# Optimization experiments

Hardware: AMD Instinct MI355X
Metric: run time of the kernel (lower is better)

Reference implementation:

```python
import jax, jax.numpy as jnp
import numpy as np

FEATURES_DIM = 100000
NUM_FIELDS = 39
EMBED_DIM = 64
DIM_INT = (2, 3)
RANK = (32, 32)
BATCH = 8192


def setup_inputs() -> dict:
    key = jax.random.key(0)
    ks = jax.random.split(key, 6)
    x = jax.random.randint(ks[0], (BATCH, NUM_FIELDS), 0, FEATURES_DIM)
    embed_table = jax.random.normal(ks[1], (FEATURES_DIM, EMBED_DIM), dtype=jnp.float32) * 0.01
    linear_w = jax.random.normal(ks[2], (FEATURES_DIM, 1), dtype=jnp.float32) * 0.01
    linear_bias = jnp.zeros((1,), dtype=jnp.float32)
    # trunc_normal_(std=0.01) approximated by clipped normal
    W0 = jnp.clip(jax.random.normal(ks[3], (DIM_INT[0], RANK[0], NUM_FIELDS), dtype=jnp.float32) * 0.01, -0.02, 0.02)
    W1 = jnp.clip(jax.random.normal(ks[4], (DIM_INT[1], RANK[1], NUM_FIELDS), dtype=jnp.float32) * 0.01, -0.02, 0.02)
    return {"x": x, "embed_table": embed_table, "linear_w": linear_w,
            "linear_bias": linear_bias, "W0": W0, "W1": W1}


def _calc_cross(W, emb):
    # W: (l, j, k) = (dim_int, rank, num_fields); emb: (b, k, i) = (batch, fields, embed)
    # dot_products[b,i,j,l] = sum_k W[l,j,k] * emb[b,k,i]
    dp = jnp.einsum('ljk,bki->bijl', W, emb)          # (b, embed, rank, dim_int)
    prod_over_l = jnp.prod(dp, axis=3)                # (b, embed, rank)
    return jnp.sum(prod_over_l, axis=(1, 2))          # (b,)


def reference(x, embed_table, linear_w, linear_bias, W0, W1):
    emb = embed_table[x]                              # (b, fields, embed)
    lin = jnp.sum(linear_w[x], axis=1) + linear_bias  # (b, 1)
    ret = lin[:, 0] + _calc_cross(W0, emb) + _calc_cross(W1, emb)
    return ret                                        # (b,)
```

## Files before the change

### kernel.cpp

```cpp
#include <hip/hip_runtime.h>
#include <hip/hip_bf16.h>

#define BATCH    8192
#define NF       39
#define ED       64
#define RANK     32
#define KST      72
#define NFRAG    15

typedef _Float16 half8  __attribute__((ext_vector_type(8)));
typedef float    f32x16 __attribute__((ext_vector_type(16)));

__global__ void prep_w(const float* __restrict__ W0,
                       const float* __restrict__ W1,
                       half8* __restrict__ wsW) {
    int d = blockIdx.x * 256 + threadIdx.x;
    if (d >= NFRAG * 64) return;
    int fid  = d >> 6;
    int lane = d & 63;
    int l = fid / 3, kc = fid % 3;
    int j = lane & 31, kh = lane >> 5;
    const float* base = (l < 2) ? (W0 + (l * RANK + j) * NF)
                                : (W1 + ((l - 2) * RANK + j) * NF);
    half8 h;
#pragma unroll
    for (int e = 0; e < 8; ++e) {
        int k = kc * 16 + kh * 8 + e;
        h[e] = (k < NF) ? (_Float16)base[k] : (_Float16)0.0f;
    }
    wsW[d] = h;
}

__global__ __launch_bounds__(256, 3) void tfm_kernel(
    const int*   __restrict__ x,
    const float* __restrict__ embed,
    const float* __restrict__ linw,
    const float* __restrict__ lbias,
    const half8* __restrict__ wsW,
    float*       __restrict__ out)
{
    __shared__ __align__(16) _Float16 Ws[NFRAG * 64 * 8];
    __shared__ __align__(16) _Float16 Ef[4][ED][KST];

    const int t    = threadIdx.x;
    const int lane = t & 63;
    const int w    = t >> 6;
    const int s    = blockIdx.x * 4 + w;

    const int j  = lane & 31;
    const int kh = lane >> 5;

    const int xi_v = (lane < NF) ? x[s * NF + lane] : 0;
    const float lv = (lane < NF) ? linw[xi_v] : 0.0f;

    float r[NF];
#pragma unroll
    for (int k = 0; k < NF; ++k) {
        int xi = __builtin_amdgcn_readlane(xi_v, k);
        r[k] = embed[(size_t)xi * ED + lane];
    }

    {
        const uint4* src = (const uint4*)wsW;
        uint4*       dst = (uint4*)Ws;
#pragma unroll
        for (int i = 0; i < NFRAG * 64 / 256; ++i)
            dst[i * 256 + t] = src[i * 256 + t];
        if (t < NFRAG * 64 - 768) dst[768 + t] = src[768 + t];
    }

    const float bias = lbias[0];

#pragma unroll
    for (int c6 = 0; c6 < 6; ++c6) {
        half8 hh;
#pragma unroll
        for (int e = 0; e < 8; ++e) {
            int k = c6 * 8 + e;
            hh[e] = (k < NF) ? (_Float16)r[k] : (_Float16)0.0f;
        }
        *(half8*)&Ef[w][lane][c6 * 8] = hh;
    }

    __syncthreads();

    const half8* Wf = (const half8*)Ws;
    float ssum = lv;

#pragma unroll
    for (int tile = 0; tile < 2; ++tile) {
        const int c = tile * 32 + j;
        half8 bf[3];
#pragma unroll
        for (int kc = 0; kc < 3; ++kc)
            bf[kc] = *(const half8*)&Ef[w][c][kc * 16 + kh * 8];

        {
            f32x16 a0, a1;
#pragma unroll
            for (int e = 0; e < 16; ++e) { a0[e] = 0.0f; a1[e] = 0.0f; }
#pragma unroll
            for (int kc = 0; kc < 3; ++kc) {
                a0 = __builtin_amdgcn_mfma_f32_32x32x16_f16(Wf[(0 * 3 + kc) * 64 + lane], bf[kc], a0, 0, 0, 0);
                a1 = __builtin_amdgcn_mfma_f32_32x32x16_f16(Wf[(1 * 3 + kc) * 64 + lane], bf[kc], a1, 0, 0, 0);
            }
#pragma unroll
            for (int e = 0; e < 16; ++e) ssum += a0[e] * a1[e];
        }
        {
            f32x16 c0, c1, c2;
#pragma unroll
            for (int e = 0; e < 16; ++e) { c0[e] = 0.0f; c1[e] = 0.0f; c2[e] = 0.0f; }
#pragma unroll
            for (int kc = 0; kc < 3; ++kc) {
                c0 = __builtin_amdgcn_mfma_f32_32x32x16_f16(Wf[(2 * 3 + kc) * 64 + lane], bf[kc], c0, 0, 0, 0);
                c1 = __builtin_amdgcn_mfma_f32_32x32x16_f16(Wf[(3 * 3 + kc) * 64 + lane], bf[kc], c1, 0, 0, 0);
                c2 = __builtin_amdgcn_mfma_f32_32x32x16_f16(Wf[(4 * 3 + kc) * 64 + lane], bf[kc], c2, 0, 0, 0);
            }
#pragma unroll
            for (int e = 0; e < 16; ++e) ssum += c0[e] * c1[e] * c2[e];
        }
    }

#pragma unroll
    for (int off = 32; off > 0; off >>= 1) ssum += __shfl_down(ssum, off, 64);
    if (lane == 0) out[s] = ssum + bias;
}

extern "C" void kernel_launch(void* const* d_in, const int* in_sizes, int n_in,
                              void* d_out, int out_size, void* d_ws, size_t ws_size,
                              hipStream_t stream) {
    const int*   x     = (const int*)  d_in[0];
    const float* embed = (const float*)d_in[1];
    const float* linw  = (const float*)d_in[2];
    const float* lbias = (const float*)d_in[3];
    const float* W0    = (const float*)d_in[4];
    const float* W1    = (const float*)d_in[5];
    float*       out   = (float*)d_out;
    half8*       wsW   = (half8*)d_ws;

    prep_w<<<(NFRAG * 64 + 255) / 256, 256, 0, stream>>>(W0, W1, wsW);
    tfm_kernel<<<BATCH / 4, 256, 0, stream>>>(x, embed, linw, lbias, wsW, out);
}
```

Before: 95.56 us.

## Fuse weight prep into main kernel, shrink LDS stride, raise occupancy

Removes the separate prep_w launch: each block now converts W0/W1 to fp16 MFMA fragments directly in shared memory. Embedding row indices are loaded as scalar (uniform) values instead of readlane broadcasts, the Ef row stride shrinks from 72 to 40 halves, the last K chunk is zero-masked in registers, and the product reductions are split into four independent accumulators. Launch bounds move to 4 blocks per CU. The intent is to drop one kernel launch, cut LDS use so more blocks fit per CU, and shorten dependency chains, at the cost of every block redoing the weight conversion from global memory.

```diff
diff --git a/kernel.cpp b/kernel.cpp
--- a/kernel.cpp
+++ b/kernel.cpp
@@ -1,42 +1,22 @@
 #include <hip/hip_runtime.h>
-#include <hip/hip_bf16.h>
 
 #define BATCH    8192
 #define NF       39
 #define ED       64
 #define RANK     32
-#define KST      72
+#define KST      40
 #define NFRAG    15
 
 typedef _Float16 half8  __attribute__((ext_vector_type(8)));
 typedef float    f32x16 __attribute__((ext_vector_type(16)));
 
-__global__ void prep_w(const float* __restrict__ W0,
-                       const float* __restrict__ W1,
-                       half8* __restrict__ wsW) {
-    int d = blockIdx.x * 256 + threadIdx.x;
-    if (d >= NFRAG * 64) return;
-    int fid  = d >> 6;
-    int lane = d & 63;
-    int l = fid / 3, kc = fid % 3;
-    int j = lane & 31, kh = lane >> 5;
-    const float* base = (l < 2) ? (W0 + (l * RANK + j) * NF)
-                                : (W1 + ((l - 2) * RANK + j) * NF);
-    half8 h;
-#pragma unroll
-    for (int e = 0; e < 8; ++e) {
-        int k = kc * 16 + kh * 8 + e;
-        h[e] = (k < NF) ? (_Float16)base[k] : (_Float16)0.0f;
-    }
-    wsW[d] = h;
-}
-
-__global__ __launch_bounds__(256, 3) void tfm_kernel(
+__global__ __launch_bounds__(256, 4) void tfm_kernel(
     const int*   __restrict__ x,
     const float* __restrict__ embed,
     const float* __restrict__ linw,
     const float* __restrict__ lbias,
-    const half8* __restrict__ wsW,
+    const float* __restrict__ W0,
+    const float* __restrict__ W1,
     float*       __restrict__ out)
 {
     __shared__ __align__(16) _Float16 Ws[NFRAG * 64 * 8];
@@ -45,55 +25,73 @@
     const int t    = threadIdx.x;
     const int lane = t & 63;
     const int w    = t >> 6;
-    const int s    = blockIdx.x * 4 + w;
+    const int s    = __builtin_amdgcn_readfirstlane(blockIdx.x * 4 + w);
 
-    const int j  = lane & 31;
-    const int kh = lane >> 5;
+    const int* __restrict__ xrow = x + s * NF;
+    int xi[NF];
+#pragma unroll
+    for (int k = 0; k < NF; ++k) xi[k] = xrow[k];
 
-    const int xi_v = (lane < NF) ? x[s * NF + lane] : 0;
-    const float lv = (lane < NF) ? linw[xi_v] : 0.0f;
+    const int   xi_v = (lane < NF) ? x[s * NF + lane] : 0;
+    const float lv   = (lane < NF) ? linw[xi_v] : 0.0f;
+    const float bias = lbias[0];
+
+#pragma unroll
+    for (int pass = 0; pass < 4; ++pass) {
+        int d = pass * 256 + t;
+        if (pass < 3 || d < NFRAG * 64) {
+            int fid = d >> 6, dl = d & 63;
+            int l = fid / 3, kc = fid % 3;
+            int j = dl & 31, kh2 = dl >> 5;
+            const float* base = (l < 2) ? (W0 + (l * RANK + j) * NF)
+                                        : (W1 + ((l - 2) * RANK + j) * NF);
+            half8 h;
+#pragma unroll
+            for (int e = 0; e < 8; ++e) {
+                int k = kc * 16 + kh2 * 8 + e;
+                h[e] = (k < NF) ? (_Float16)base[k] : (_Float16)0.0f;
+            }
+            *(half8*)&Ws[d * 8] = h;
+        }
+    }
 
     float r[NF];
 #pragma unroll
-    for (int k = 0; k < NF; ++k) {
-        int xi = __builtin_amdgcn_readlane(xi_v, k);
-        r[k] = embed[(size_t)xi * ED + lane];
-    }
-
-    {
-        const uint4* src = (const uint4*)wsW;
-        uint4*       dst = (uint4*)Ws;
-#pragma unroll
-        for (int i = 0; i < NFRAG * 64 / 256; ++i)
-            dst[i * 256 + t] = src[i * 256 + t];
-        if (t < NFRAG * 64 - 768) dst[768 + t] = src[768 + t];
-    }
-
-    const float bias = lbias[0];
+    for (int k = 0; k < NF; ++k)
+        r[k] = embed[(size_t)xi[k] * ED + lane];
 
 #pragma unroll
-    for (int c6 = 0; c6 < 6; ++c6) {
+    for (int c5 = 0; c5 < 5; ++c5) {
         half8 hh;
 #pragma unroll
         for (int e = 0; e < 8; ++e) {
-            int k = c6 * 8 + e;
+            int k = c5 * 8 + e;
             hh[e] = (k < NF) ? (_Float16)r[k] : (_Float16)0.0f;
         }
-        *(half8*)&Ef[w][lane][c6 * 8] = hh;
+        *(half8*)&Ef[w][lane][c5 * 8] = hh;
     }
 
     __syncthreads();
 
     const half8* Wf = (const half8*)Ws;
+    const int j  = lane & 31;
+    const int kh = lane >> 5;
     float ssum = lv;
+
+    half8 hz;
+#pragma unroll
+    for (int e = 0; e < 8; ++e) hz[e] = (_Float16)0.0f;
 
 #pragma unroll
     for (int tile = 0; tile < 2; ++tile) {
         const int c = tile * 32 + j;
         half8 bf[3];
-#pragma unroll
-        for (int kc = 0; kc < 3; ++kc)
-            bf[kc] = *(const half8*)&Ef[w][c][kc * 16 + kh * 8];
+        bf[0] = *(const half8*)&Ef[w][c][kh * 8];
+        bf[1] = *(const half8*)&Ef[w][c][16 + kh * 8];
+        {
+            half8 b2 = *(const half8*)&Ef[w][c][32];
+            bf[2] = kh ? hz : b2;
+        }
 
         {
             f32x16 a0, a1;
@@ -104,8 +102,15 @@
                 a0 = __builtin_amdgcn_mfma_f32_32x32x16_f16(Wf[(0 * 3 + kc) * 64 + lane], bf[kc], a0, 0, 0, 0);
                 a1 = __builtin_amdgcn_mfma_f32_32x32x16_f16(Wf[(1 * 3 + kc) * 64 + lane], bf[kc], a1, 0, 0, 0);
             }
+            float p0 = 0.f, p1 = 0.f, p2 = 0.f, p3 = 0.f;
 #pragma unroll
-            for (int e = 0; e < 16; ++e) ssum += a0[e] * a1[e];
+            for (int e = 0; e < 4; ++e) {
+                p0 += a0[e]      * a1[e];
+                p1 += a0[4 + e]  * a1[4 + e];
+                p2 += a0[8 + e]  * a1[8 + e];
+                p3 += a0[12 + e] * a1[12 + e];
+            }
+            ssum += (p0 + p1) + (p2 + p3);
         }
         {
             f32x16 c0, c1, c2;
@@ -117,8 +122,15 @@
                 c1 = __builtin_amdgcn_mfma_f32_32x32x16_f16(Wf[(3 * 3 + kc) * 64 + lane], bf[kc], c1, 0, 0, 0);
                 c2 = __builtin_amdgcn_mfma_f32_32x32x16_f16(Wf[(4 * 3 + kc) * 64 + lane], bf[kc], c2, 0, 0, 0);
             }
+            float q0 = 0.f, q1 = 0.f, q2 = 0.f, q3 = 0.f;
 #pragma unroll
-            for (int e = 0; e < 16; ++e) ssum += c0[e] * c1[e] * c2[e];
+            for (int e = 0; e < 4; ++e) {
+                q0 += c0[e]      * c1[e]      * c2[e];
+                q1 += c0[4 + e]  * c1[4 + e]  * c2[4 + e];
+                q2 += c0[8 + e]  * c1[8 + e]  * c2[8 + e];
+                q3 += c0[12 + e] * c1[12 + e] * c2[12 + e];
+            }
+            ssum += (q0 + q1) + (q2 + q3);
         }
     }
 
@@ -137,8 +149,6 @@
     const float* W0    = (const float*)d_in[4];
     const float* W1    = (const float*)d_in[5];
     float*       out   = (float*)d_out;
-    half8*       wsW   = (half8*)d_ws;
 
-    prep_w<<<(NFRAG * 64 + 255) / 256, 256, 0, stream>>>(W0, W1, wsW);
-    tfm_kernel<<<BATCH / 4, 256, 0, stream>>>(x, embed, linw, lbias, wsW, out);
+    tfm_kernel<<<BATCH / 4, 256, 0, stream>>>(x, embed, linw, lbias, W0, W1, out);
 }
```

Result: slower. 103.2 us (+8.0%).
